# Optimization experiments

Measured on AMD Instinct MI355X. Metric: run time of the kernel, lower is better.

The kernel has to match this reference:

```python
import math
import jax, jax.numpy as jnp
import numpy as np

EPS = 1e-5
B, S, D = 2, 2048, 2048
Z, HD, H, N = 512, 4096, 8, 8
ZH, VH = Z // H, HD // H  # 64, 512
GROUPS = 32


def timestep_norm(x, w, b):
    # cumulative (over time) group normalization; groups of dg channels
    dg = D // GROUPS
    xg = x.reshape(B, S, GROUPS, dg)
    s1 = jnp.cumsum(xg.sum(-1), axis=1)                 # [B,S,G]
    s2 = jnp.cumsum(jnp.square(xg).sum(-1), axis=1)     # [B,S,G]
    cnt = (jnp.arange(S, dtype=x.dtype) + 1.0) * dg
    mean = s1 / cnt[None, :, None]
    var = s2 / cnt[None, :, None] - jnp.square(mean)
    xn = (xg - mean[..., None]) * jax.lax.rsqrt(var[..., None] + EPS)
    return xn.reshape(B, S, D) * w + b


def cema(x, alpha, delta, theta, gamma, omega):
    # complex multi-head EMA: h_t = a*e^{i\theta} x_t + (1-a*d)*e^{i\theta} h_{t-1};
    # y_t = Re(gamma^H h_t) + omega * x_t    (real-arithmetic form, scan over time)
    p = jax.nn.sigmoid(alpha)                      # [D,N]
    qm = 1.0 - p * jax.nn.sigmoid(delta)           # [D,N]
    phase = jax.nn.sigmoid(theta)[:, None] * (2.0 * math.pi * (jnp.arange(N, dtype=x.dtype) + 1.0) / N)
    c, s = jnp.cos(phase), jnp.sin(phase)
    ur, ui = p * c, p * s
    qr, qi = qm * c, qm * s
    gr, gi = gamma[..., 0], gamma[..., 1]

    def step(h, xt):  # xt: [B,D]
        hr, hi = h
        nhr = qr * hr - qi * hi + ur * xt[..., None]
        nhi = qi * hr + qr * hi + ui * xt[..., None]
        y = jnp.sum(nhr * gr + nhi * gi, axis=-1)  # [B,D]
        return (nhr, nhi), y

    h0 = (jnp.zeros((B, D, N), x.dtype), jnp.zeros((B, D, N), x.dtype))
    _, ys = jax.lax.scan(step, h0, jnp.moveaxis(x, 1, 0))
    return jnp.moveaxis(ys, 0, 1) + x * omega


def rmsnorm(x, w=None):
    y = x * jax.lax.rsqrt(jnp.mean(jnp.square(x), axis=-1, keepdims=True) + EPS)
    return y if w is None else y * w


def apply_rotary(xq, xk, freqs):
    # xq/xk: [B,S,H,ZH]; freqs: [S, ZH//2, 2] (cos, sin)
    cos = freqs[None, :, None, :, 0]
    sin = freqs[None, :, None, :, 1]

    def rot(x):
        xr = x.reshape(*x.shape[:-1], ZH // 2, 2)
        re, im = xr[..., 0], xr[..., 1]
        out = jnp.stack([re * cos - im * sin, re * sin + im * cos], axis=-1)
        return out.reshape(x.shape)

    return rot(xq), rot(xk)


def setup_inputs():
    key = jax.random.key(0)
    ks = jax.random.split(key, 24)
    p = 0.02
    inp = {
        "x": jax.random.normal(ks[0], (B, S, D), jnp.float32),
        "tn_weight": 1.0 + p * jax.random.normal(ks[1], (D,), jnp.float32),
        "tn_bias": p * jax.random.normal(ks[2], (D,), jnp.float32),
        "ema_alpha": jax.random.normal(ks[3], (D, N), jnp.float32),
        "ema_delta": jax.random.normal(ks[4], (D, N), jnp.float32),
        "ema_theta": jax.random.normal(ks[5], (D,), jnp.float32),
        "ema_gamma": jax.random.normal(ks[6], (D, N, 2), jnp.float32) / math.sqrt(N),
        "ema_omega": p * jax.random.normal(ks[7], (D,), jnp.float32),
        "rms_weight": 1.0 + p * jax.random.normal(ks[8], (D,), jnp.float32),
        "wz_w": jax.random.normal(ks[9], (D, Z), jnp.float32) / math.sqrt(D),
        "wz_b": p * jax.random.normal(ks[10], (Z,), jnp.float32),
        "wv_w": jax.random.normal(ks[11], (D, HD), jnp.float32) / math.sqrt(D),
        "wv_b": p * jax.random.normal(ks[12], (HD,), jnp.float32),
        "wr_w": jax.random.normal(ks[13], (D, HD), jnp.float32) / math.sqrt(D),
        "wr_b": p * jax.random.normal(ks[14], (HD,), jnp.float32),
        "wh1_w": jax.random.normal(ks[15], (D, D), jnp.float32) / math.sqrt(D),
        "wh1_b": p * jax.random.normal(ks[16], (D,), jnp.float32),
        "wh2_w": jax.random.normal(ks[17], (HD, D), jnp.float32) / math.sqrt(HD),
        "attn_gamma": p * jax.random.normal(ks[18], (2, Z), jnp.float32),
        "attn_beta": p * jax.random.normal(ks[19], (2, Z), jnp.float32),
    }
    # rotary freqs (cos, sin) for head dim ZH
    inv = 1.0 / (10000.0 ** (np.arange(0, ZH, 2, dtype=np.float32) / ZH))
    ang = np.arange(S, dtype=np.float32)[:, None] * inv[None, :]
    inp["freqs_cis"] = jnp.asarray(np.stack([np.cos(ang), np.sin(ang)], axis=-1))
    return inp


def reference(x, freqs_cis, tn_weight, tn_bias, ema_alpha, ema_delta, ema_theta,
              ema_gamma, ema_omega, rms_weight, wz_w, wz_b, wv_w, wv_b, wr_w, wr_b,
              wh1_w, wh1_b, wh2_w, attn_gamma, attn_beta):
    residual = x
    out_tsn = timestep_norm(x, tn_weight, tn_bias)
    out_cema = cema(out_tsn, ema_alpha, ema_delta, ema_theta, ema_gamma, ema_omega)
    mx = rmsnorm(out_cema, rms_weight)

    z = mx @ wz_w + wz_b                              # [B,S,Z]
    z = rmsnorm(z.reshape(B, S, H, ZH)).reshape(B, S, Z)
    gamma = (attn_gamma + 1.0) / math.sqrt(ZH)        # [2,Z]
    z2 = z[:, :, None, :] * gamma + attn_beta         # [B,S,2,Z]
    q, k = z2[:, :, 0], z2[:, :, 1]

    v = jax.nn.silu(out_tsn @ wv_w + wv_b)            # [B,S,HD]
    r = jax.nn.silu(mx @ wr_w + wr_b)                 # [B,S,HD]

    qh = q.reshape(B, S, H, ZH)
    kh = k.reshape(B, S, H, ZH)
    vh = v.reshape(B, S, H, VH)
    qh, kh = apply_rotary(qh, kh, freqs_cis)

    # causal additive mask; scale 1.0 (folded into gamma)
    neg = jnp.finfo(jnp.float32).min
    mask = jnp.where(jnp.tril(jnp.ones((S, S), bool)), 0.0, neg).astype(jnp.float32)
    scores = jnp.einsum('bqhd,bkhd->bhqk', qh, kh) + mask
    probs = jax.nn.softmax(scores.astype(jnp.float32), axis=-1).astype(qh.dtype)
    attn = jnp.einsum('bhqk,bkhd->bqhd', probs, vh).reshape(B, S, HD)

    attn = attn * r
    h = (mx @ wh1_w + wh1_b) + attn @ wh2_w
    return h + residual
```

## Files before the change

### kernel.cpp

```cpp
#include <hip/hip_runtime.h>
#include <stdint.h>


typedef __bf16 bf16_t;
typedef bf16_t bf16x8 __attribute__((ext_vector_type(8)));
typedef float floatx4 __attribute__((ext_vector_type(4)));
typedef __attribute__((address_space(1))) unsigned int as1_uint;
typedef __attribute__((address_space(3))) unsigned int as3_uint;

static constexpr int kB = 2, kS = 2048, kD = 2048;
static constexpr int kZ = 512, kHD = 4096, kH = 8;
static constexpr int kG = 32;
static constexpr int kC = 64, kL = 32;

__device__ __forceinline__ void async16(void* lds, const void* g) {
  __builtin_amdgcn_global_load_lds((const as1_uint*)(size_t)g, (as3_uint*)lds, 16, 0, 0);
}

__device__ __forceinline__ float sigm(float x) { return 1.0f / (1.0f + expf(-x)); }

__global__ __launch_bounds__(256) void wtrans_kernel(const float* __restrict__ W,
                                                     bf16_t* __restrict__ Wt,
                                                     int K, int N, int ldWt,
                                                     int colOff) {
  __shared__ float tile[32][33];
  int n0 = blockIdx.x * 32, k0 = blockIdx.y * 32;
  int tx = threadIdx.x & 31, ty = threadIdx.x >> 5;
#pragma unroll
  for (int i = 0; i < 32; i += 8)
    tile[ty + i][tx] = W[(size_t)(k0 + ty + i) * N + n0 + tx];
  __syncthreads();
#pragma unroll
  for (int i = 0; i < 32; i += 8)
    Wt[(size_t)(n0 + ty + i) * ldWt + colOff + k0 + tx] = (bf16_t)tile[tx][ty + i];
}

__global__ __launch_bounds__(256) void tsn_sums(const float* __restrict__ x,
                                                float* __restrict__ g1,
                                                float* __restrict__ g2) {
  int bs = blockIdx.x, t = threadIdx.x;
  const float4* rp = (const float4*)(x + (size_t)bs * kD + t * 8);
  float4 a = rp[0], b = rp[1];
  float s1 = a.x + a.y + a.z + a.w + b.x + b.y + b.z + b.w;
  float s2 = a.x * a.x + a.y * a.y + a.z * a.z + a.w * a.w +
             b.x * b.x + b.y * b.y + b.z * b.z + b.w * b.w;
  s1 += __shfl_xor(s1, 1); s2 += __shfl_xor(s2, 1);
  s1 += __shfl_xor(s1, 2); s2 += __shfl_xor(s2, 2);
  s1 += __shfl_xor(s1, 4); s2 += __shfl_xor(s2, 4);
  if ((t & 7) == 0) {
    int g = t >> 3, b_ = bs >> 11, s = bs & 2047;
    size_t idx = ((size_t)b_ * kG + g) * kS + s;
    g1[idx] = s1; g2[idx] = s2;
  }
}

__global__ void tsn_scan(float* __restrict__ g1, float* __restrict__ g2) {
  int lane = threadIdx.x;
  size_t base = (size_t)blockIdx.x * kS;
  float c1 = 0.f, c2 = 0.f;
  for (int c = 0; c < kS / 64; ++c) {
    size_t idx = base + c * 64 + lane;
    float v1 = g1[idx], v2 = g2[idx];
#pragma unroll
    for (int off = 1; off < 64; off <<= 1) {
      float t1 = __shfl_up(v1, off), t2 = __shfl_up(v2, off);
      if (lane >= off) { v1 += t1; v2 += t2; }
    }
    v1 += c1; v2 += c2;
    g1[idx] = v1; g2[idx] = v2;
    c1 = __shfl(v1, 63); c2 = __shfl(v2, 63);
  }
}

__global__ __launch_bounds__(256) void tsn_norm(const float* __restrict__ x,
    const float* __restrict__ g1, const float* __restrict__ g2,
    const float* __restrict__ w, const float* __restrict__ bias,
    float* __restrict__ tsn, bf16_t* __restrict__ tsnb) {
  int bs = blockIdx.x, t = threadIdx.x;
  int b = bs >> 11, s = bs & 2047, g = t >> 3;
  float cnt = (float)(s + 1) * 64.0f;
  size_t gidx = ((size_t)b * kG + g) * kS + s;
  float mean = g1[gidx] / cnt;
  float inv = rsqrtf(g2[gidx] / cnt - mean * mean + 1e-5f);
  size_t base = (size_t)bs * kD + t * 8;
  float4 a = ((const float4*)(x + base))[0];
  float4 c = ((const float4*)(x + base))[1];
  float v[8] = {a.x, a.y, a.z, a.w, c.x, c.y, c.z, c.w};
  float4 w0 = ((const float4*)(w + t * 8))[0], w1 = ((const float4*)(w + t * 8))[1];
  float4 b0 = ((const float4*)(bias + t * 8))[0], b1 = ((const float4*)(bias + t * 8))[1];
  float wv[8] = {w0.x, w0.y, w0.z, w0.w, w1.x, w1.y, w1.z, w1.w};
  float bv[8] = {b0.x, b0.y, b0.z, b0.w, b1.x, b1.y, b1.z, b1.w};
  float r[8];
  bf16x8 ob;
#pragma unroll
  for (int i = 0; i < 8; ++i) {
    r[i] = (v[i] - mean) * inv * wv[i] + bv[i];
    ob[i] = (bf16_t)r[i];
  }
  ((float4*)(tsn + base))[0] = make_float4(r[0], r[1], r[2], r[3]);
  ((float4*)(tsn + base))[1] = make_float4(r[4], r[5], r[6], r[7]);
  *(bf16x8*)(tsnb + base) = ob;
}

__device__ __forceinline__ void cema_coeffs(const float* __restrict__ alpha,
    const float* __restrict__ delta, float st, int d,
    float (&qr)[8], float (&qi)[8], float (&ur)[8], float (&ui)[8]) {
  const float4* ap = (const float4*)(alpha + (size_t)d * 8);
  const float4* dp = (const float4*)(delta + (size_t)d * 8);
  float4 a0 = ap[0], a1 = ap[1], d0 = dp[0], d1 = dp[1];
  float av[8] = {a0.x, a0.y, a0.z, a0.w, a1.x, a1.y, a1.z, a1.w};
  float dv[8] = {d0.x, d0.y, d0.z, d0.w, d1.x, d1.y, d1.z, d1.w};
#pragma unroll
  for (int n = 0; n < 8; ++n) {
    float p = sigm(av[n]);
    float qm = 1.0f - p * sigm(dv[n]);
    float ph = st * (0.78539816339744831f * (float)(n + 1));
    float cs = cosf(ph), sn = sinf(ph);
    qr[n] = qm * cs; qi[n] = qm * sn;
    ur[n] = p * cs;  ui[n] = p * sn;
  }
}

__global__ __launch_bounds__(256) void cema_pass1(const float* __restrict__ tsn,
    const float* __restrict__ alpha, const float* __restrict__ delta,
    const float* __restrict__ theta, float2* __restrict__ hend) {
  int b = blockIdx.x >> 6, c = blockIdx.x & 63;
  int d = blockIdx.y * 256 + threadIdx.x;
  float st = sigm(theta[d]);
  float qr[8], qi[8], ur[8], ui[8];
  cema_coeffs(alpha, delta, st, d, qr, qi, ur, ui);
  float hr[8] = {0}, hi[8] = {0};
  const float* xp = tsn + ((size_t)b * kS + c * kL) * kD + d;
  for (int i = 0; i < kL; ++i) {
    float xt = xp[(size_t)i * kD];
#pragma unroll
    for (int n = 0; n < 8; ++n) {
      float tr = fmaf(qr[n], hr[n], fmaf(-qi[n], hi[n], ur[n] * xt));
      float ti = fmaf(qi[n], hr[n], fmaf(qr[n], hi[n], ui[n] * xt));
      hr[n] = tr; hi[n] = ti;
    }
  }
  float2* op = hend + (((size_t)(b * kC + c)) * kD + d) * 8;
#pragma unroll
  for (int n = 0; n < 8; ++n) op[n] = make_float2(hr[n], hi[n]);
}

__global__ __launch_bounds__(256) void cema_pass2(const float2* __restrict__ hend,
    const float* __restrict__ alpha, const float* __restrict__ delta,
    const float* __restrict__ theta, float2* __restrict__ hinit) {
  int tid = blockIdx.x * 256 + threadIdx.x;
  int n = tid & 7, d = (tid >> 3) & 2047, b = tid >> 14;
  int dn = d * 8 + n;
  float p = sigm(alpha[dn]);
  float qm = 1.0f - p * sigm(delta[dn]);
  float ph = sigm(theta[d]) * (0.78539816339744831f * (float)(n + 1));
  float ar = qm * cosf(ph), ai = qm * sinf(ph);
#pragma unroll
  for (int t = 0; t < 5; ++t) {
    float nr = ar * ar - ai * ai;
    ai = 2.0f * ar * ai;
    ar = nr;
  }
  float hr = 0.f, hi = 0.f;
  for (int c = 0; c < kC; ++c) {
    size_t idx = (((size_t)(b * kC + c)) * kD + d) * 8 + n;
    hinit[idx] = make_float2(hr, hi);
    float2 e = hend[idx];
    float nr = fmaf(ar, hr, fmaf(-ai, hi, e.x));
    float ni = fmaf(ai, hr, fmaf(ar, hi, e.y));
    hr = nr; hi = ni;
  }
}

__global__ __launch_bounds__(256) void cema_pass3(const float* __restrict__ tsn,
    const float* __restrict__ alpha, const float* __restrict__ delta,
    const float* __restrict__ theta, const float* __restrict__ gamma,
    const float* __restrict__ omega, const float2* __restrict__ hinit,
    float* __restrict__ outc) {
  int b = blockIdx.x >> 6, c = blockIdx.x & 63;
  int d = blockIdx.y * 256 + threadIdx.x;
  float st = sigm(theta[d]);
  float qr[8], qi[8], ur[8], ui[8];
  cema_coeffs(alpha, delta, st, d, qr, qi, ur, ui);
  float gr[8], gi[8];
  const float4* gp = (const float4*)(gamma + (size_t)d * 16);
#pragma unroll
  for (int m = 0; m < 4; ++m) {
    float4 g = gp[m];
    gr[m * 2] = g.x; gi[m * 2] = g.y; gr[m * 2 + 1] = g.z; gi[m * 2 + 1] = g.w;
  }
  float om = omega[d];
  float hr[8], hi[8];
  const float2* ip = hinit + (((size_t)(b * kC + c)) * kD + d) * 8;
#pragma unroll
  for (int n = 0; n < 8; ++n) { float2 h = ip[n]; hr[n] = h.x; hi[n] = h.y; }
  const float* xp = tsn + ((size_t)b * kS + c * kL) * kD + d;
  float* op = outc + ((size_t)b * kS + c * kL) * kD + d;
  for (int i = 0; i < kL; ++i) {
    float xt = xp[(size_t)i * kD];
    float y = 0.f;
#pragma unroll
    for (int n = 0; n < 8; ++n) {
      float tr = fmaf(qr[n], hr[n], fmaf(-qi[n], hi[n], ur[n] * xt));
      float ti = fmaf(qi[n], hr[n], fmaf(qr[n], hi[n], ui[n] * xt));
      hr[n] = tr; hi[n] = ti;
      y = fmaf(tr, gr[n], fmaf(ti, gi[n], y));
    }
    op[(size_t)i * kD] = fmaf(xt, om, y);
  }
}

__global__ __launch_bounds__(256) void rms_kernel(const float* __restrict__ in,
                                                  const float* __restrict__ w,
                                                  bf16_t* __restrict__ outb) {
  int bs = blockIdx.x, t = threadIdx.x;
  size_t base = (size_t)bs * kD + t * 8;
  float4 a = ((const float4*)(in + base))[0];
  float4 c = ((const float4*)(in + base))[1];
  float v[8] = {a.x, a.y, a.z, a.w, c.x, c.y, c.z, c.w};
  float ss = 0.f;
#pragma unroll
  for (int i = 0; i < 8; ++i) ss += v[i] * v[i];
#pragma unroll
  for (int off = 1; off < 64; off <<= 1) ss += __shfl_xor(ss, off);
  __shared__ float red[4];
  if ((t & 63) == 0) red[t >> 6] = ss;
  __syncthreads();
  ss = red[0] + red[1] + red[2] + red[3];
  float inv = rsqrtf(ss * (1.0f / 2048.0f) + 1e-5f);
  float4 w0 = ((const float4*)(w + t * 8))[0], w1 = ((const float4*)(w + t * 8))[1];
  float wv[8] = {w0.x, w0.y, w0.z, w0.w, w1.x, w1.y, w1.z, w1.w};
  bf16x8 ob;
#pragma unroll
  for (int i = 0; i < 8; ++i) ob[i] = (bf16_t)(v[i] * inv * wv[i]);
  *(bf16x8*)(outb + base) = ob;
}

__global__ __launch_bounds__(256) void zpost_kernel(const float* __restrict__ z,
    const float* __restrict__ ag, const float* __restrict__ ab,
    const float* __restrict__ freqs, bf16_t* __restrict__ q, bf16_t* __restrict__ k) {
  int bs = blockIdx.x, t = threadIdx.x;
  int b = bs >> 11, s = bs & 2047;
  int h = t >> 5, i = t & 31;
  const float* zr = z + (size_t)bs * kZ + h * 64;
  float re = zr[2 * i], im = zr[2 * i + 1];
  float ss = re * re + im * im;
#pragma unroll
  for (int off = 1; off < 32; off <<= 1) ss += __shfl_xor(ss, off);
  float inv = rsqrtf(ss * (1.0f / 64.0f) + 1e-5f);
  float zne = re * inv, zno = im * inv;
  const float rs = 0.125f;
  int ze = h * 64 + 2 * i, zo = ze + 1;
  float qe = zne * ((ag[ze] + 1.f) * rs) + ab[ze];
  float qo = zno * ((ag[zo] + 1.f) * rs) + ab[zo];
  float ke = zne * ((ag[kZ + ze] + 1.f) * rs) + ab[kZ + ze];
  float ko = zno * ((ag[kZ + zo] + 1.f) * rs) + ab[kZ + zo];
  float cs = freqs[((size_t)s * 32 + i) * 2 + 0];
  float sn = freqs[((size_t)s * 32 + i) * 2 + 1];
  size_t o = (((size_t)b * kH + h) * kS + s) * 64 + 2 * i;
  q[o]     = (bf16_t)(qe * cs - qo * sn);
  q[o + 1] = (bf16_t)(qe * sn + qo * cs);
  k[o]     = (bf16_t)(ke * cs - ko * sn);
  k[o + 1] = (bf16_t)(ke * sn + ko * cs);
}

__global__ __launch_bounds__(256) void gemm_fused3(
    const bf16_t* __restrict__ tsnb, const bf16_t* __restrict__ mx,
    const bf16_t* __restrict__ wvT, const bf16_t* __restrict__ wrT,
    const bf16_t* __restrict__ wzT, const float* __restrict__ wv_b,
    const float* __restrict__ wr_b, const float* __restrict__ wz_b,
    bf16_t* __restrict__ vTb, bf16_t* __restrict__ rb,
    float* __restrict__ zbuf) {
  __shared__ __align__(16) bf16_t sA[2][128 * 32];
  __shared__ __align__(16) bf16_t sB[2][128 * 32];
  const int bid = blockIdx.x;
  const bf16_t* A; const bf16_t* Bt; const float* bias;
  int N, epi, sub;
  if (bid < 1024)      { sub = bid;        A = tsnb; Bt = wvT; bias = wv_b; N = kHD; epi = 1; }
  else if (bid < 2048) { sub = bid - 1024; A = mx;   Bt = wrT; bias = wr_b; N = kHD; epi = 2; }
  else                 { sub = bid - 2048; A = mx;   Bt = wzT; bias = wz_b; N = kZ;  epi = 0; }
  const int m0 = (sub & 31) * 128, n0 = (sub >> 5) * 128;
  const int t = threadIdx.x;
  const int wave = t >> 6, lane = t & 63;
  const int quad = lane >> 4, l16 = lane & 15;
  const int wm = (wave >> 1) * 64, wn = (wave & 1) * 64;
  const int K = kD;

  floatx4 acc[4][4];
#pragma unroll
  for (int i = 0; i < 4; ++i)
#pragma unroll
    for (int j = 0; j < 4; ++j) acc[i][j] = (floatx4){0.f, 0.f, 0.f, 0.f};

  const int seg0 = wave * 64 + lane;
  const int seg1 = 256 + wave * 64 + lane;
  const int r0 = seg0 >> 2, c0 = (seg0 & 3) * 8;
  const int r1 = seg1 >> 2, c1 = (seg1 & 3) * 8;

  auto stage = [&](int buf, int kt) {
    async16(sA[buf] + (size_t)(wave * 64) * 8,       A + (size_t)(m0 + r0) * K + kt + c0);
    async16(sA[buf] + (size_t)(256 + wave * 64) * 8, A + (size_t)(m0 + r1) * K + kt + c1);
    async16(sB[buf] + (size_t)(wave * 64) * 8,       Bt + (size_t)(n0 + r0) * K + kt + c0);
    async16(sB[buf] + (size_t)(256 + wave * 64) * 8, Bt + (size_t)(n0 + r1) * K + kt + c1);
  };

  stage(0, 0);
  __syncthreads();

  const int nsteps = K >> 5;
  for (int st = 0; st < nsteps; ++st) {
    const int cur = st & 1;
    if (st + 1 < nsteps) stage(cur ^ 1, (st + 1) << 5);

    bf16x8 af[4], bfr[4];
#pragma unroll
    for (int i = 0; i < 4; ++i)
      af[i] = *(const bf16x8*)(sA[cur] + (wm + i * 16 + l16) * 32 + quad * 8);
#pragma unroll
    for (int j = 0; j < 4; ++j)
      bfr[j] = *(const bf16x8*)(sB[cur] + (wn + j * 16 + l16) * 32 + quad * 8);
#pragma unroll
    for (int i = 0; i < 4; ++i)
#pragma unroll
      for (int j = 0; j < 4; ++j)
        acc[i][j] = __builtin_amdgcn_mfma_f32_16x16x32_bf16(af[i], bfr[j], acc[i][j], 0, 0, 0);

    __syncthreads();
  }

#pragma unroll
  for (int i = 0; i < 4; ++i) {
#pragma unroll
    for (int j = 0; j < 4; ++j) {
#pragma unroll
      for (int r = 0; r < 4; ++r) {
        int row = m0 + wm + i * 16 + quad * 4 + r;
        int col = n0 + wn + j * 16 + l16;
        size_t idx = (size_t)row * N + col;
        float v = acc[i][j][r];
        if (epi == 0) {
          zbuf[idx] = v + bias[col];
        } else if (epi == 1) {
          v += bias[col];
          v = v / (1.f + __expf(-v));
          size_t vidx = ((size_t)(row >> 11) * kHD + col) * (size_t)kS + (row & 2047);
          vTb[vidx] = (bf16_t)v;
        } else {
          v += bias[col];
          v = v / (1.f + __expf(-v));
          rb[idx] = (bf16_t)v;
        }
      }
    }
  }
}

__global__ __launch_bounds__(256) void gemm_bt(const bf16_t* __restrict__ A1,
    int lda1, const bf16_t* __restrict__ A2, int lda2, int K1,
    const bf16_t* __restrict__ Bt, int M, int N, int K,
    const float* __restrict__ bias, const float* __restrict__ add1,
    float* __restrict__ outF) {
  __shared__ __align__(16) bf16_t sA[2][128 * 32];
  __shared__ __align__(16) bf16_t sB[2][128 * 32];
  const int t = threadIdx.x;
  const int wave = t >> 6, lane = t & 63;
  const int quad = lane >> 4, l16 = lane & 15;
  const int m0 = blockIdx.x * 128, n0 = blockIdx.y * 128;
  const int wm = (wave >> 1) * 64, wn = (wave & 1) * 64;

  floatx4 acc[4][4];
#pragma unroll
  for (int i = 0; i < 4; ++i)
#pragma unroll
    for (int j = 0; j < 4; ++j) acc[i][j] = (floatx4){0.f, 0.f, 0.f, 0.f};

  const int seg0 = wave * 64 + lane;
  const int seg1 = 256 + wave * 64 + lane;
  const int r0 = seg0 >> 2, c0 = (seg0 & 3) * 8;
  const int r1 = seg1 >> 2, c1 = (seg1 & 3) * 8;

  auto stage = [&](int buf, int kt) {
    const bf16_t* Ab; int ldab; int kk;
    if (kt < K1) { Ab = A1; ldab = lda1; kk = kt; }
    else         { Ab = A2; ldab = lda2; kk = kt - K1; }
    async16(sA[buf] + (size_t)(wave * 64) * 8,       Ab + (size_t)(m0 + r0) * ldab + kk + c0);
    async16(sA[buf] + (size_t)(256 + wave * 64) * 8, Ab + (size_t)(m0 + r1) * ldab + kk + c1);
    async16(sB[buf] + (size_t)(wave * 64) * 8,       Bt + (size_t)(n0 + r0) * K + kt + c0);
    async16(sB[buf] + (size_t)(256 + wave * 64) * 8, Bt + (size_t)(n0 + r1) * K + kt + c1);
  };

  stage(0, 0);
  __syncthreads();

  const int nsteps = K >> 5;
  for (int st = 0; st < nsteps; ++st) {
    const int cur = st & 1;
    if (st + 1 < nsteps) stage(cur ^ 1, (st + 1) << 5);

    bf16x8 af[4], bfr[4];
#pragma unroll
    for (int i = 0; i < 4; ++i)
      af[i] = *(const bf16x8*)(sA[cur] + (wm + i * 16 + l16) * 32 + quad * 8);
#pragma unroll
    for (int j = 0; j < 4; ++j)
      bfr[j] = *(const bf16x8*)(sB[cur] + (wn + j * 16 + l16) * 32 + quad * 8);
#pragma unroll
    for (int i = 0; i < 4; ++i)
#pragma unroll
      for (int j = 0; j < 4; ++j)
        acc[i][j] = __builtin_amdgcn_mfma_f32_16x16x32_bf16(af[i], bfr[j], acc[i][j], 0, 0, 0);

    __syncthreads();
  }

#pragma unroll
  for (int i = 0; i < 4; ++i) {
#pragma unroll
    for (int j = 0; j < 4; ++j) {
#pragma unroll
      for (int r = 0; r < 4; ++r) {
        int row = m0 + wm + i * 16 + quad * 4 + r;
        int col = n0 + wn + j * 16 + l16;
        size_t idx = (size_t)row * N + col;
        outF[idx] = acc[i][j][r] + bias[col] + add1[idx];
      }
    }
  }
}

__global__ __launch_bounds__(256) void attn_kernel(const bf16_t* __restrict__ qg,
    const bf16_t* __restrict__ kg, const bf16_t* __restrict__ vT,
    const bf16_t* __restrict__ rg, bf16_t* __restrict__ attnG) {
  const int bid = blockIdx.x;
  const int qt = (kS / 64 - 1) - (bid >> 5);
  const int bh = (bid >> 1) & 15;
  const int vs = bid & 1;
  const int b = bh >> 3, h = bh & 7;
  const int t = threadIdx.x;
  const int w = t >> 6, lane = t & 63;
  const int quad = lane >> 4, l16 = lane & 15;
  const int q0 = qt * 64;

  __shared__ __align__(16) bf16_t sP[2][64 * 64];
  __shared__ __align__(16) bf16_t sK[2][64 * 64];
  __shared__ float sM[64], sL[64], sAl[2][64];
  if (t < 64) { sM[t] = 0.f; sL[t] = 0.f; }

  const bf16_t* qbase = qg + ((size_t)bh * kS + q0) * 64;
  const bf16_t* kbase = kg + (size_t)bh * kS * 64;
  const bf16_t* vbase = vT + ((size_t)bh * 512 + vs * 256 + w * 64) * kS;

  auto stage_k = [&](bf16_t* dstbuf, int k0) {
#pragma unroll
    for (int half = 0; half < 2; ++half) {
      int seg = half * 256 + w * 64 + lane;
      int r = seg >> 3, cc = seg & 7;
      async16(dstbuf + (size_t)(half * 256 + w * 64) * 8,
              kbase + (size_t)(k0 + r) * 64 + (cc ^ (r & 7)) * 8);
    }
  };

  bf16x8 qfrag[2];
#pragma unroll
  for (int ks = 0; ks < 2; ++ks)
    qfrag[ks] = *(const bf16x8*)(qbase + (size_t)(w * 16 + l16) * 64 + ks * 32 + quad * 8);

  floatx4 oacc[4][4];
#pragma unroll
  for (int i = 0; i < 4; ++i)
#pragma unroll
    for (int j = 0; j < 4; ++j) oacc[i][j] = (floatx4){0.f, 0.f, 0.f, 0.f};

  stage_k(sK[0], 0);
  __syncthreads();

  for (int kt = 0; kt <= qt; ++kt) {
    const int k0 = kt * 64;
    const int pb = kt & 1;

    if (kt < qt) stage_k(sK[pb ^ 1], k0 + 64);

    bf16x8 vf[2][4];
#pragma unroll
    for (int ks = 0; ks < 2; ++ks)
#pragma unroll
      for (int nj = 0; nj < 4; ++nj)
        vf[ks][nj] = *(const bf16x8*)(vbase + (size_t)(nj * 16 + l16) * kS + k0 + ks * 32 + quad * 8);

    floatx4 sacc[4];
#pragma unroll
    for (int nt = 0; nt < 4; ++nt) sacc[nt] = (floatx4){0.f, 0.f, 0.f, 0.f};
#pragma unroll
    for (int ks = 0; ks < 2; ++ks)
#pragma unroll
      for (int nt = 0; nt < 4; ++nt) {
        int row = nt * 16 + l16;
        int ch = (ks * 4 + quad) ^ (row & 7);
        bf16x8 kf = *(const bf16x8*)(sK[pb] + row * 64 + ch * 8);
        sacc[nt] = __builtin_amdgcn_mfma_f32_16x16x32_bf16(qfrag[ks], kf, sacc[nt], 0, 0, 0);
      }
    if (kt == qt) {
#pragma unroll
      for (int nt = 0; nt < 4; ++nt)
#pragma unroll
        for (int r = 0; r < 4; ++r) {
          int sk = k0 + nt * 16 + l16;
          int qq = q0 + w * 16 + quad * 4 + r;
          if (sk > qq) sacc[nt][r] = -1e30f;
        }
    }

    float mo[4], mloc[4], lspec[4];
#pragma unroll
    for (int r = 0; r < 4; ++r) {
      mo[r] = sM[w * 16 + quad * 4 + r];
      mloc[r] = fmaxf(fmaxf(sacc[0][r], sacc[1][r]), fmaxf(sacc[2][r], sacc[3][r]));
    }
#pragma unroll
    for (int r = 0; r < 4; ++r) {
      float s = 0.f;
#pragma unroll
      for (int nt = 0; nt < 4; ++nt) {
        float e = __expf(sacc[nt][r] - mo[r]);
        sacc[nt][r] = e;
        s += e;
      }
      lspec[r] = s;
    }
#pragma unroll
    for (int off = 1; off < 16; off <<= 1)
#pragma unroll
      for (int r = 0; r < 4; ++r) {
        mloc[r] = fmaxf(mloc[r], __shfl_xor(mloc[r], off));
        lspec[r] += __shfl_xor(lspec[r], off);
      }
    float mnew[4], al[4];
#pragma unroll
    for (int r = 0; r < 4; ++r) {
      mnew[r] = fmaxf(mo[r], mloc[r]);
      al[r] = __expf(mo[r] - mnew[r]);
    }
    if (l16 == 0) {
#pragma unroll
      for (int r = 0; r < 4; ++r) {
        int row = w * 16 + quad * 4 + r;
        sM[row] = mnew[r];
        sL[row] = al[r] * (sL[row] + lspec[r]);
        sAl[pb][row] = al[r];
      }
    }
#pragma unroll
    for (int nt = 0; nt < 4; ++nt)
#pragma unroll
      for (int r = 0; r < 4; ++r) {
        int row = w * 16 + quad * 4 + r;
        sP[pb][row * 64 + ((nt * 16 + l16) ^ ((row & 7) << 3))] = (bf16_t)(sacc[nt][r] * al[r]);
      }

    __syncthreads();

#pragma unroll
    for (int mi = 0; mi < 4; ++mi)
#pragma unroll
      for (int r = 0; r < 4; ++r) {
        float a = sAl[pb][mi * 16 + quad * 4 + r];
#pragma unroll
        for (int nj = 0; nj < 4; ++nj) oacc[mi][nj][r] *= a;
      }
    __builtin_amdgcn_s_setprio(1);
#pragma unroll
    for (int ks = 0; ks < 2; ++ks) {
      bf16x8 pa[4];
#pragma unroll
      for (int mi = 0; mi < 4; ++mi) {
        int row = mi * 16 + l16;
        pa[mi] = *(const bf16x8*)(sP[pb] + row * 64 + ((ks * 32 + quad * 8) ^ ((row & 7) << 3)));
      }
#pragma unroll
      for (int nj = 0; nj < 4; ++nj)
#pragma unroll
        for (int mi = 0; mi < 4; ++mi)
          oacc[mi][nj] = __builtin_amdgcn_mfma_f32_16x16x32_bf16(pa[mi], vf[ks][nj], oacc[mi][nj], 0, 0, 0);
    }
    __builtin_amdgcn_s_setprio(0);
  }

#pragma unroll
  for (int mi = 0; mi < 4; ++mi)
#pragma unroll
    for (int r = 0; r < 4; ++r) {
      int srow = q0 + mi * 16 + quad * 4 + r;
      float linv = 1.0f / sL[mi * 16 + quad * 4 + r];
#pragma unroll
      for (int nj = 0; nj < 4; ++nj) {
        int hd = h * 512 + vs * 256 + w * 64 + nj * 16 + l16;
        size_t idx = ((size_t)b * kS + srow) * kHD + hd;
        float rv = (float)rg[idx];
        attnG[idx] = (bf16_t)(oacc[mi][nj][r] * linv * rv);
      }
    }
}

extern "C" void kernel_launch(void* const* d_in, const int* in_sizes, int n_in,
                              void* d_out, int out_size, void* d_ws, size_t ws_size,
                              hipStream_t stream) {
  const float* x      = (const float*)d_in[0];
  const float* tnw    = (const float*)d_in[1];
  const float* tnb    = (const float*)d_in[2];
  const float* ealpha = (const float*)d_in[3];
  const float* edelta = (const float*)d_in[4];
  const float* etheta = (const float*)d_in[5];
  const float* egamma = (const float*)d_in[6];
  const float* eomega = (const float*)d_in[7];
  const float* rmsw   = (const float*)d_in[8];
  const float* wz_w   = (const float*)d_in[9];
  const float* wz_b   = (const float*)d_in[10];
  const float* wv_w   = (const float*)d_in[11];
  const float* wv_b   = (const float*)d_in[12];
  const float* wr_w   = (const float*)d_in[13];
  const float* wr_b   = (const float*)d_in[14];
  const float* wh1_w  = (const float*)d_in[15];
  const float* wh1_b  = (const float*)d_in[16];
  const float* wh2_w  = (const float*)d_in[17];
  const float* ag     = (const float*)d_in[18];
  const float* ab     = (const float*)d_in[19];
  const float* freqs  = (const float*)d_in[20];
  float* out = (float*)d_out;

  char* ws = (char*)d_ws;
  size_t off = 0;
  auto alloc = [&](size_t bytes) -> void* {
    void* p = ws + off;
    off += (bytes + 255) & ~(size_t)255;
    return p;
  };
  float*  tsn  = (float*)alloc(8388608ull * 4);
  bf16_t* tsnb = (bf16_t*)alloc(8388608ull * 2);
  float*  g1   = (float*)alloc(131072ull * 4);
  float*  g2   = (float*)alloc(131072ull * 4);
  float*  cema = (float*)alloc(8388608ull * 4);
  bf16_t* mx   = (bf16_t*)alloc(8388608ull * 2);
  bf16_t* wzT  = (bf16_t*)alloc(1048576ull * 2);
  bf16_t* wvT  = (bf16_t*)alloc(8388608ull * 2);
  bf16_t* wrT  = (bf16_t*)alloc(8388608ull * 2);
  bf16_t* whcT = (bf16_t*)alloc(12582912ull * 2);
  float*  zbuf = (float*)alloc(2097152ull * 4);
  bf16_t* qb   = (bf16_t*)alloc(2097152ull * 2);
  bf16_t* kb   = (bf16_t*)alloc(2097152ull * 2);
  bf16_t* rb   = (bf16_t*)alloc(16777216ull * 2);
  bf16_t* aG   = (bf16_t*)alloc(16777216ull * 2);
  bf16_t* vTb  = (bf16_t*)tsn;
  float*  h1   = cema;
  float2* hend  = (float2*)rb;
  float2* hinit = (float2*)aG;
  (void)h1;

  wtrans_kernel<<<dim3(kZ / 32, kD / 32), 256, 0, stream>>>(wz_w, wzT, kD, kZ, kD, 0);
  wtrans_kernel<<<dim3(kHD / 32, kD / 32), 256, 0, stream>>>(wv_w, wvT, kD, kHD, kD, 0);
  wtrans_kernel<<<dim3(kHD / 32, kD / 32), 256, 0, stream>>>(wr_w, wrT, kD, kHD, kD, 0);
  wtrans_kernel<<<dim3(kD / 32, kD / 32), 256, 0, stream>>>(wh1_w, whcT, kD, kD, 6144, 0);
  wtrans_kernel<<<dim3(kD / 32, kHD / 32), 256, 0, stream>>>(wh2_w, whcT, kHD, kD, 6144, kD);

  tsn_sums<<<kB * kS, 256, 0, stream>>>(x, g1, g2);
  tsn_scan<<<kB * kG, 64, 0, stream>>>(g1, g2);
  tsn_norm<<<kB * kS, 256, 0, stream>>>(x, g1, g2, tnw, tnb, tsn, tsnb);

  cema_pass1<<<dim3(kB * kC, kD / 256), 256, 0, stream>>>(tsn, ealpha, edelta,
                                                          etheta, hend);
  cema_pass2<<<kB * kD * 8 / 256, 256, 0, stream>>>(hend, ealpha, edelta,
                                                    etheta, hinit);
  cema_pass3<<<dim3(kB * kC, kD / 256), 256, 0, stream>>>(tsn, ealpha, edelta,
      etheta, egamma, eomega, hinit, cema);
  rms_kernel<<<kB * kS, 256, 0, stream>>>(cema, rmsw, mx);

  const int M = kB * kS;
  gemm_fused3<<<dim3(2176), 256, 0, stream>>>(tsnb, mx, wvT, wrT, wzT,
      wv_b, wr_b, wz_b, vTb, rb, zbuf);
  zpost_kernel<<<kB * kS, 256, 0, stream>>>(zbuf, ag, ab, freqs, qb, kb);
  attn_kernel<<<dim3(1024), 256, 0, stream>>>(qb, kb, vTb, rb, aG);
  gemm_bt<<<dim3(M / 128, kD / 128), 256, 0, stream>>>(mx, kD, aG, kHD, kD,
      whcT, M, kD, 6144, wh1_b, x, out);
  (void)in_sizes; (void)n_in; (void)out_size; (void)ws_size;
}
```

Baseline: 872.4 us.

## Move wh1 GEMM into fused projection launch and split attention over more blocks

Moves the mx@wh1 part of the output projection into the fused projection GEMM launch as an extra 512 blocks. Those blocks write bias plus residual plus the partial product to a float buffer. The final GEMM then only has to do the K=4096 attn@wh2 product and add that partial. The attention kernel now splits each head's value dimension into 4 slices instead of 2, so it launches 2048 blocks with fewer output accumulators each. The aim is better occupancy and load balance and a shorter serial tail for the last GEMM, at the cost of extra fp32 partial traffic and recomputing QK^T/softmax across more V slices.

```diff
diff --git a/kernel.cpp b/kernel.cpp
--- a/kernel.cpp
+++ b/kernel.cpp
@@ -264,21 +264,24 @@
   k[o + 1] = (bf16_t)(ke * sn + ko * cs);
 }
 
-__global__ __launch_bounds__(256) void gemm_fused3(
+__global__ __launch_bounds__(256) void gemm_fused4(
     const bf16_t* __restrict__ tsnb, const bf16_t* __restrict__ mx,
     const bf16_t* __restrict__ wvT, const bf16_t* __restrict__ wrT,
-    const bf16_t* __restrict__ wzT, const float* __restrict__ wv_b,
-    const float* __restrict__ wr_b, const float* __restrict__ wz_b,
+    const bf16_t* __restrict__ wzT, const bf16_t* __restrict__ whcT,
+    const float* __restrict__ wv_b, const float* __restrict__ wr_b,
+    const float* __restrict__ wz_b, const float* __restrict__ wh1_b,
+    const float* __restrict__ x,
     bf16_t* __restrict__ vTb, bf16_t* __restrict__ rb,
-    float* __restrict__ zbuf) {
+    float* __restrict__ zbuf, float* __restrict__ Pw0) {
   __shared__ __align__(16) bf16_t sA[2][128 * 32];
   __shared__ __align__(16) bf16_t sB[2][128 * 32];
   const int bid = blockIdx.x;
   const bf16_t* A; const bf16_t* Bt; const float* bias;
-  int N, epi, sub;
-  if (bid < 1024)      { sub = bid;        A = tsnb; Bt = wvT; bias = wv_b; N = kHD; epi = 1; }
-  else if (bid < 2048) { sub = bid - 1024; A = mx;   Bt = wrT; bias = wr_b; N = kHD; epi = 2; }
-  else                 { sub = bid - 2048; A = mx;   Bt = wzT; bias = wz_b; N = kZ;  epi = 0; }
+  int N, epi, sub, ldb;
+  if (bid < 1024)      { sub = bid;        A = tsnb; Bt = wvT;  bias = wv_b;  N = kHD; epi = 1; ldb = kD; }
+  else if (bid < 2048) { sub = bid - 1024; A = mx;   Bt = wrT;  bias = wr_b;  N = kHD; epi = 2; ldb = kD; }
+  else if (bid < 2176) { sub = bid - 2048; A = mx;   Bt = wzT;  bias = wz_b;  N = kZ;  epi = 0; ldb = kD; }
+  else                 { sub = bid - 2176; A = mx;   Bt = whcT; bias = wh1_b; N = kD;  epi = 3; ldb = 6144; }
   const int m0 = (sub & 31) * 128, n0 = (sub >> 5) * 128;
   const int t = threadIdx.x;
   const int wave = t >> 6, lane = t & 63;
@@ -300,8 +303,8 @@
   auto stage = [&](int buf, int kt) {
     async16(sA[buf] + (size_t)(wave * 64) * 8,       A + (size_t)(m0 + r0) * K + kt + c0);
     async16(sA[buf] + (size_t)(256 + wave * 64) * 8, A + (size_t)(m0 + r1) * K + kt + c1);
-    async16(sB[buf] + (size_t)(wave * 64) * 8,       Bt + (size_t)(n0 + r0) * K + kt + c0);
-    async16(sB[buf] + (size_t)(256 + wave * 64) * 8, Bt + (size_t)(n0 + r1) * K + kt + c1);
+    async16(sB[buf] + (size_t)(wave * 64) * 8,       Bt + (size_t)(n0 + r0) * ldb + kt + c0);
+    async16(sB[buf] + (size_t)(256 + wave * 64) * 8, Bt + (size_t)(n0 + r1) * ldb + kt + c1);
   };
 
   stage(0, 0);
@@ -345,20 +348,194 @@
           v = v / (1.f + __expf(-v));
           size_t vidx = ((size_t)(row >> 11) * kHD + col) * (size_t)kS + (row & 2047);
           vTb[vidx] = (bf16_t)v;
-        } else {
+        } else if (epi == 2) {
           v += bias[col];
           v = v / (1.f + __expf(-v));
           rb[idx] = (bf16_t)v;
+        } else {
+          Pw0[idx] = v + bias[col] + x[idx];
         }
       }
     }
   }
 }
 
-__global__ __launch_bounds__(256) void gemm_bt(const bf16_t* __restrict__ A1,
-    int lda1, const bf16_t* __restrict__ A2, int lda2, int K1,
-    const bf16_t* __restrict__ Bt, int M, int N, int K,
-    const float* __restrict__ bias, const float* __restrict__ add1,
+__global__ __launch_bounds__(256) void attn_kernel(const bf16_t* __restrict__ qg,
+    const bf16_t* __restrict__ kg, const bf16_t* __restrict__ vT,
+    const bf16_t* __restrict__ rg, bf16_t* __restrict__ attnG) {
+  const int bid = blockIdx.x;
+  const int qt = (kS / 64 - 1) - (bid >> 6);
+  const int sub = bid & 63;
+  const int bh = sub >> 2;
+  const int vs = sub & 3;
+  const int b = bh >> 3, h = bh & 7;
+  const int t = threadIdx.x;
+  const int w = t >> 6, lane = t & 63;
+  const int quad = lane >> 4, l16 = lane & 15;
+  const int q0 = qt * 64;
+
+  __shared__ __align__(16) bf16_t sP[2][64 * 64];
+  __shared__ __align__(16) bf16_t sK[2][64 * 64];
+  __shared__ float sM[64], sL[64], sAl[2][64];
+  if (t < 64) { sM[t] = 0.f; sL[t] = 0.f; }
+
+  const bf16_t* qbase = qg + ((size_t)bh * kS + q0) * 64;
+  const bf16_t* kbase = kg + (size_t)bh * kS * 64;
+  const bf16_t* vbase = vT + ((size_t)bh * 512 + vs * 128 + w * 32) * kS;
+
+  auto stage_k = [&](bf16_t* dstbuf, int k0) {
+#pragma unroll
+    for (int half = 0; half < 2; ++half) {
+      int seg = half * 256 + w * 64 + lane;
+      int r = seg >> 3, cc = seg & 7;
+      async16(dstbuf + (size_t)(half * 256 + w * 64) * 8,
+              kbase + (size_t)(k0 + r) * 64 + (cc ^ (r & 7)) * 8);
+    }
+  };
+
+  bf16x8 qfrag[2];
+#pragma unroll
+  for (int ks = 0; ks < 2; ++ks)
+    qfrag[ks] = *(const bf16x8*)(qbase + (size_t)(w * 16 + l16) * 64 + ks * 32 + quad * 8);
+
+  floatx4 oacc[4][2];
+#pragma unroll
+  for (int i = 0; i < 4; ++i)
+#pragma unroll
+    for (int j = 0; j < 2; ++j) oacc[i][j] = (floatx4){0.f, 0.f, 0.f, 0.f};
+
+  stage_k(sK[0], 0);
+  __syncthreads();
+
+  for (int kt = 0; kt <= qt; ++kt) {
+    const int k0 = kt * 64;
+    const int pb = kt & 1;
+
+    if (kt < qt) stage_k(sK[pb ^ 1], k0 + 64);
+
+    bf16x8 vf[2][2];
+#pragma unroll
+    for (int ks = 0; ks < 2; ++ks)
+#pragma unroll
+      for (int nj = 0; nj < 2; ++nj)
+        vf[ks][nj] = *(const bf16x8*)(vbase + (size_t)(nj * 16 + l16) * kS + k0 + ks * 32 + quad * 8);
+
+    floatx4 sacc[4];
+#pragma unroll
+    for (int nt = 0; nt < 4; ++nt) sacc[nt] = (floatx4){0.f, 0.f, 0.f, 0.f};
+#pragma unroll
+    for (int ks = 0; ks < 2; ++ks)
+#pragma unroll
+      for (int nt = 0; nt < 4; ++nt) {
+        int row = nt * 16 + l16;
+        int ch = (ks * 4 + quad) ^ (row & 7);
+        bf16x8 kf = *(const bf16x8*)(sK[pb] + row * 64 + ch * 8);
+        sacc[nt] = __builtin_amdgcn_mfma_f32_16x16x32_bf16(qfrag[ks], kf, sacc[nt], 0, 0, 0);
+      }
+    if (kt == qt) {
+#pragma unroll
+      for (int nt = 0; nt < 4; ++nt)
+#pragma unroll
+        for (int r = 0; r < 4; ++r) {
+          int sk = k0 + nt * 16 + l16;
+          int qq = q0 + w * 16 + quad * 4 + r;
+          if (sk > qq) sacc[nt][r] = -1e30f;
+        }
+    }
+
+    float mo[4], mloc[4], lspec[4];
+#pragma unroll
+    for (int r = 0; r < 4; ++r) {
+      mo[r] = sM[w * 16 + quad * 4 + r];
+      mloc[r] = fmaxf(fmaxf(sacc[0][r], sacc[1][r]), fmaxf(sacc[2][r], sacc[3][r]));
+    }
+#pragma unroll
+    for (int r = 0; r < 4; ++r) {
+      float s = 0.f;
+#pragma unroll
+      for (int nt = 0; nt < 4; ++nt) {
+        float e = __expf(sacc[nt][r] - mo[r]);
+        sacc[nt][r] = e;
+        s += e;
+      }
+      lspec[r] = s;
+    }
+#pragma unroll
+    for (int off = 1; off < 16; off <<= 1)
+#pragma unroll
+      for (int r = 0; r < 4; ++r) {
+        mloc[r] = fmaxf(mloc[r], __shfl_xor(mloc[r], off));
+        lspec[r] += __shfl_xor(lspec[r], off);
+      }
+    float mnew[4], al[4];
+#pragma unroll
+    for (int r = 0; r < 4; ++r) {
+      mnew[r] = fmaxf(mo[r], mloc[r]);
+      al[r] = __expf(mo[r] - mnew[r]);
+    }
+    if (l16 == 0) {
+#pragma unroll
+      for (int r = 0; r < 4; ++r) {
+        int row = w * 16 + quad * 4 + r;
+        sM[row] = mnew[r];
+        sL[row] = al[r] * (sL[row] + lspec[r]);
+        sAl[pb][row] = al[r];
+      }
+    }
+#pragma unroll
+    for (int nt = 0; nt < 4; ++nt)
+#pragma unroll
+      for (int r = 0; r < 4; ++r) {
+        int row = w * 16 + quad * 4 + r;
+        sP[pb][row * 64 + ((nt * 16 + l16) ^ ((row & 7) << 3))] = (bf16_t)(sacc[nt][r] * al[r]);
+      }
+
+    __syncthreads();
+
+#pragma unroll
+    for (int mi = 0; mi < 4; ++mi)
+#pragma unroll
+      for (int r = 0; r < 4; ++r) {
+        float a = sAl[pb][mi * 16 + quad * 4 + r];
+#pragma unroll
+        for (int nj = 0; nj < 2; ++nj) oacc[mi][nj][r] *= a;
+      }
+    __builtin_amdgcn_s_setprio(1);
+#pragma unroll
+    for (int ks = 0; ks < 2; ++ks) {
+      bf16x8 pa[4];
+#pragma unroll
+      for (int mi = 0; mi < 4; ++mi) {
+        int row = mi * 16 + l16;
+        pa[mi] = *(const bf16x8*)(sP[pb] + row * 64 + ((ks * 32 + quad * 8) ^ ((row & 7) << 3)));
+      }
+#pragma unroll
+      for (int nj = 0; nj < 2; ++nj)
+#pragma unroll
+        for (int mi = 0; mi < 4; ++mi)
+          oacc[mi][nj] = __builtin_amdgcn_mfma_f32_16x16x32_bf16(pa[mi], vf[ks][nj], oacc[mi][nj], 0, 0, 0);
+    }
+    __builtin_amdgcn_s_setprio(0);
+  }
+
+#pragma unroll
+  for (int mi = 0; mi < 4; ++mi)
+#pragma unroll
+    for (int r = 0; r < 4; ++r) {
+      int srow = q0 + mi * 16 + quad * 4 + r;
+      float linv = 1.0f / sL[mi * 16 + quad * 4 + r];
+#pragma unroll
+      for (int nj = 0; nj < 2; ++nj) {
+        int hd = h * 512 + vs * 128 + w * 32 + nj * 16 + l16;
+        size_t idx = ((size_t)b * kS + srow) * kHD + hd;
+        float rv = (float)rg[idx];
+        attnG[idx] = (bf16_t)(oacc[mi][nj][r] * linv * rv);
+      }
+    }
+}
+
+__global__ __launch_bounds__(256) void gemm_final(const bf16_t* __restrict__ aG,
+    const bf16_t* __restrict__ whcT, const float* __restrict__ Pw0,
     float* __restrict__ outF) {
   __shared__ __align__(16) bf16_t sA[2][128 * 32];
   __shared__ __align__(16) bf16_t sB[2][128 * 32];
@@ -367,6 +544,7 @@
   const int quad = lane >> 4, l16 = lane & 15;
   const int m0 = blockIdx.x * 128, n0 = blockIdx.y * 128;
   const int wm = (wave >> 1) * 64, wn = (wave & 1) * 64;
+  const int N = kD, K = kHD, lda = kHD, ldB = 6144, cOff = 2048;
 
   floatx4 acc[4][4];
 #pragma unroll
@@ -380,13 +558,10 @@
   const int r1 = seg1 >> 2, c1 = (seg1 & 3) * 8;
 
   auto stage = [&](int buf, int kt) {
-    const bf16_t* Ab; int ldab; int kk;
-    if (kt < K1) { Ab = A1; ldab = lda1; kk = kt; }
-    else         { Ab = A2; ldab = lda2; kk = kt - K1; }
-    async16(sA[buf] + (size_t)(wave * 64) * 8,       Ab + (size_t)(m0 + r0) * ldab + kk + c0);
-    async16(sA[buf] + (size_t)(256 + wave * 64) * 8, Ab + (size_t)(m0 + r1) * ldab + kk + c1);
-    async16(sB[buf] + (size_t)(wave * 64) * 8,       Bt + (size_t)(n0 + r0) * K + kt + c0);
-    async16(sB[buf] + (size_t)(256 + wave * 64) * 8, Bt + (size_t)(n0 + r1) * K + kt + c1);
+    async16(sA[buf] + (size_t)(wave * 64) * 8,       aG + (size_t)(m0 + r0) * lda + kt + c0);
+    async16(sA[buf] + (size_t)(256 + wave * 64) * 8, aG + (size_t)(m0 + r1) * lda + kt + c1);
+    async16(sB[buf] + (size_t)(wave * 64) * 8,       whcT + (size_t)(n0 + r0) * ldB + cOff + kt + c0);
+    async16(sB[buf] + (size_t)(256 + wave * 64) * 8, whcT + (size_t)(n0 + r1) * ldB + cOff + kt + c1);
   };
 
   stage(0, 0);
@@ -414,191 +589,16 @@
   }
 
 #pragma unroll
-  for (int i = 0; i < 4; ++i) {
-#pragma unroll
-    for (int j = 0; j < 4; ++j) {
+  for (int i = 0; i < 4; ++i)
+#pragma unroll
+    for (int j = 0; j < 4; ++j)
 #pragma unroll
       for (int r = 0; r < 4; ++r) {
         int row = m0 + wm + i * 16 + quad * 4 + r;
         int col = n0 + wn + j * 16 + l16;
         size_t idx = (size_t)row * N + col;
-        outF[idx] = acc[i][j][r] + bias[col] + add1[idx];
-      }
-    }
-  }
-}
-
-__global__ __launch_bounds__(256) void attn_kernel(const bf16_t* __restrict__ qg,
-    const bf16_t* __restrict__ kg, const bf16_t* __restrict__ vT,
-    const bf16_t* __restrict__ rg, bf16_t* __restrict__ attnG) {
-  const int bid = blockIdx.x;
-  const int qt = (kS / 64 - 1) - (bid >> 5);
-  const int bh = (bid >> 1) & 15;
-  const int vs = bid & 1;
-  const int b = bh >> 3, h = bh & 7;
-  const int t = threadIdx.x;
-  const int w = t >> 6, lane = t & 63;
-  const int quad = lane >> 4, l16 = lane & 15;
-  const int q0 = qt * 64;
-
-  __shared__ __align__(16) bf16_t sP[2][64 * 64];
-  __shared__ __align__(16) bf16_t sK[2][64 * 64];
-  __shared__ float sM[64], sL[64], sAl[2][64];
-  if (t < 64) { sM[t] = 0.f; sL[t] = 0.f; }
-
-  const bf16_t* qbase = qg + ((size_t)bh * kS + q0) * 64;
-  const bf16_t* kbase = kg + (size_t)bh * kS * 64;
-  const bf16_t* vbase = vT + ((size_t)bh * 512 + vs * 256 + w * 64) * kS;
-
-  auto stage_k = [&](bf16_t* dstbuf, int k0) {
-#pragma unroll
-    for (int half = 0; half < 2; ++half) {
-      int seg = half * 256 + w * 64 + lane;
-      int r = seg >> 3, cc = seg & 7;
-      async16(dstbuf + (size_t)(half * 256 + w * 64) * 8,
-              kbase + (size_t)(k0 + r) * 64 + (cc ^ (r & 7)) * 8);
-    }
-  };
-
-  bf16x8 qfrag[2];
-#pragma unroll
-  for (int ks = 0; ks < 2; ++ks)
-    qfrag[ks] = *(const bf16x8*)(qbase + (size_t)(w * 16 + l16) * 64 + ks * 32 + quad * 8);
-
-  floatx4 oacc[4][4];
-#pragma unroll
-  for (int i = 0; i < 4; ++i)
-#pragma unroll
-    for (int j = 0; j < 4; ++j) oacc[i][j] = (floatx4){0.f, 0.f, 0.f, 0.f};
-
-  stage_k(sK[0], 0);
-  __syncthreads();
-
-  for (int kt = 0; kt <= qt; ++kt) {
-    const int k0 = kt * 64;
-    const int pb = kt & 1;
-
-    if (kt < qt) stage_k(sK[pb ^ 1], k0 + 64);
-
-    bf16x8 vf[2][4];
-#pragma unroll
-    for (int ks = 0; ks < 2; ++ks)
-#pragma unroll
-      for (int nj = 0; nj < 4; ++nj)
-        vf[ks][nj] = *(const bf16x8*)(vbase + (size_t)(nj * 16 + l16) * kS + k0 + ks * 32 + quad * 8);
-
-    floatx4 sacc[4];
-#pragma unroll
-    for (int nt = 0; nt < 4; ++nt) sacc[nt] = (floatx4){0.f, 0.f, 0.f, 0.f};
-#pragma unroll
-    for (int ks = 0; ks < 2; ++ks)
-#pragma unroll
-      for (int nt = 0; nt < 4; ++nt) {
-        int row = nt * 16 + l16;
-        int ch = (ks * 4 + quad) ^ (row & 7);
-        bf16x8 kf = *(const bf16x8*)(sK[pb] + row * 64 + ch * 8);
-        sacc[nt] = __builtin_amdgcn_mfma_f32_16x16x32_bf16(qfrag[ks], kf, sacc[nt], 0, 0, 0);
-      }
-    if (kt == qt) {
-#pragma unroll
-      for (int nt = 0; nt < 4; ++nt)
-#pragma unroll
-        for (int r = 0; r < 4; ++r) {
-          int sk = k0 + nt * 16 + l16;
-          int qq = q0 + w * 16 + quad * 4 + r;
-          if (sk > qq) sacc[nt][r] = -1e30f;
-        }
-    }
-
-    float mo[4], mloc[4], lspec[4];
-#pragma unroll
-    for (int r = 0; r < 4; ++r) {
-      mo[r] = sM[w * 16 + quad * 4 + r];
-      mloc[r] = fmaxf(fmaxf(sacc[0][r], sacc[1][r]), fmaxf(sacc[2][r], sacc[3][r]));
-    }
-#pragma unroll
-    for (int r = 0; r < 4; ++r) {
-      float s = 0.f;
-#pragma unroll
-      for (int nt = 0; nt < 4; ++nt) {
-        float e = __expf(sacc[nt][r] - mo[r]);
-        sacc[nt][r] = e;
-        s += e;
-      }
-      lspec[r] = s;
-    }
-#pragma unroll
-    for (int off = 1; off < 16; off <<= 1)
-#pragma unroll
-      for (int r = 0; r < 4; ++r) {
-        mloc[r] = fmaxf(mloc[r], __shfl_xor(mloc[r], off));
-        lspec[r] += __shfl_xor(lspec[r], off);
-      }
-    float mnew[4], al[4];
-#pragma unroll
-    for (int r = 0; r < 4; ++r) {
-      mnew[r] = fmaxf(mo[r], mloc[r]);
-      al[r] = __expf(mo[r] - mnew[r]);
-    }
-    if (l16 == 0) {
-#pragma unroll
-      for (int r = 0; r < 4; ++r) {
-        int row = w * 16 + quad * 4 + r;
-        sM[row] = mnew[r];
-        sL[row] = al[r] * (sL[row] + lspec[r]);
-        sAl[pb][row] = al[r];
-      }
-    }
-#pragma unroll
-    for (int nt = 0; nt < 4; ++nt)
-#pragma unroll
-      for (int r = 0; r < 4; ++r) {
-        int row = w * 16 + quad * 4 + r;
-        sP[pb][row * 64 + ((nt * 16 + l16) ^ ((row & 7) << 3))] = (bf16_t)(sacc[nt][r] * al[r]);
-      }
-
-    __syncthreads();
-
-#pragma unroll
-    for (int mi = 0; mi < 4; ++mi)
-#pragma unroll
-      for (int r = 0; r < 4; ++r) {
-        float a = sAl[pb][mi * 16 + quad * 4 + r];
-#pragma unroll
-        for (int nj = 0; nj < 4; ++nj) oacc[mi][nj][r] *= a;
-      }
-    __builtin_amdgcn_s_setprio(1);
-#pragma unroll
-    for (int ks = 0; ks < 2; ++ks) {
-      bf16x8 pa[4];
-#pragma unroll
-      for (int mi = 0; mi < 4; ++mi) {
-        int row = mi * 16 + l16;
-        pa[mi] = *(const bf16x8*)(sP[pb] + row * 64 + ((ks * 32 + quad * 8) ^ ((row & 7) << 3)));
-      }
-#pragma unroll
-      for (int nj = 0; nj < 4; ++nj)
-#pragma unroll
-        for (int mi = 0; mi < 4; ++mi)
-          oacc[mi][nj] = __builtin_amdgcn_mfma_f32_16x16x32_bf16(pa[mi], vf[ks][nj], oacc[mi][nj], 0, 0, 0);
-    }
-    __builtin_amdgcn_s_setprio(0);
-  }
-
-#pragma unroll
-  for (int mi = 0; mi < 4; ++mi)
-#pragma unroll
-    for (int r = 0; r < 4; ++r) {
-      int srow = q0 + mi * 16 + quad * 4 + r;
-      float linv = 1.0f / sL[mi * 16 + quad * 4 + r];
-#pragma unroll
-      for (int nj = 0; nj < 4; ++nj) {
-        int hd = h * 512 + vs * 256 + w * 64 + nj * 16 + l16;
-        size_t idx = ((size_t)b * kS + srow) * kHD + hd;
-        float rv = (float)rg[idx];
-        attnG[idx] = (bf16_t)(oacc[mi][nj][r] * linv * rv);
-      }
-    }
+        outF[idx] = acc[i][j][r] + Pw0[idx];
+      }
 }
 
 extern "C" void kernel_launch(void* const* d_in, const int* in_sizes, int n_in,
@@ -650,10 +650,9 @@
   bf16_t* rb   = (bf16_t*)alloc(16777216ull * 2);
   bf16_t* aG   = (bf16_t*)alloc(16777216ull * 2);
   bf16_t* vTb  = (bf16_t*)tsn;
-  float*  h1   = cema;
+  float*  Pw0  = cema;
   float2* hend  = (float2*)rb;
   float2* hinit = (float2*)aG;
-  (void)h1;
 
   wtrans_kernel<<<dim3(kZ / 32, kD / 32), 256, 0, stream>>>(wz_w, wzT, kD, kZ, kD, 0);
   wtrans_kernel<<<dim3(kHD / 32, kD / 32), 256, 0, stream>>>(wv_w, wvT, kD, kHD, kD, 0);
@@ -674,11 +673,10 @@
   rms_kernel<<<kB * kS, 256, 0, stream>>>(cema, rmsw, mx);
 
   const int M = kB * kS;
-  gemm_fused3<<<dim3(2176), 256, 0, stream>>>(tsnb, mx, wvT, wrT, wzT,
-      wv_b, wr_b, wz_b, vTb, rb, zbuf);
+  gemm_fused4<<<dim3(2688), 256, 0, stream>>>(tsnb, mx, wvT, wrT, wzT, whcT,
+      wv_b, wr_b, wz_b, wh1_b, x, vTb, rb, zbuf, Pw0);
   zpost_kernel<<<kB * kS, 256, 0, stream>>>(zbuf, ag, ab, freqs, qb, kb);
-  attn_kernel<<<dim3(1024), 256, 0, stream>>>(qb, kb, vTb, rb, aG);
-  gemm_bt<<<dim3(M / 128, kD / 128), 256, 0, stream>>>(mx, kD, aG, kHD, kD,
-      whcT, M, kD, 6144, wh1_b, x, out);
+  attn_kernel<<<dim3(2048), 256, 0, stream>>>(qb, kb, vTb, rb, aG);
+  gemm_final<<<dim3(M / 128, kD / 128), 256, 0, stream>>>(aG, whcT, Pw0, out);
   (void)in_sizes; (void)n_in; (void)out_size; (void)ws_size;
 }
```

After: 909.7 us. 4.3% more time.
